# Performance work log

Hardware: AMD Instinct MI355X
Metric: run time of the kernel (lower is better)

The kernel has to match this reference:

```python
import jax, jax.numpy as jnp
import numpy as np

GRID = 18          # grid_dim
NTYPES = 6         # n_atom_types
SIGMA_P = 0.6      # sigma * bins_per_angstrom
B = 256            # number of environments (batch)
ATOMS_PER_ENV = 100
N = B * ATOMS_PER_ENV
EPS = 1e-5
SLOPE = 0.01       # LeakyReLU default negative slope


def _grid_points():
    # lin_spacing(): centers of 18 unit bins, -8.5 .. 8.5
    ls = np.linspace(-GRID / 2 + 0.5, GRID / 2 - 0.5, GRID)
    xx, yy, zz = np.meshgrid(ls, ls, ls, indexing='ij')
    return jnp.asarray(np.stack([xx, yy, zz], -1).reshape(-1, 3), jnp.float32)  # [G,3]


def _leaky(x):
    return jnp.where(x >= 0, x, SLOPE * x)


def _bn(x, g, b):
    # batch-norm with batch statistics (torch training-mode math), channel axis 1
    axes = tuple(i for i in range(x.ndim) if i != 1)
    m = x.mean(axes, keepdims=True)
    v = x.var(axes, keepdims=True)
    shp = [1] * x.ndim
    shp[1] = -1
    return (x - m) / jnp.sqrt(v + EPS) * g.reshape(shp) + b.reshape(shp)


def _conv3d(x, w, b, pad):
    y = jax.lax.conv_general_dilated(
        x, w, window_strides=(1, 1, 1), padding=[(pad, pad)] * 3,
        dimension_numbers=('NCDHW', 'OIDHW', 'NCDHW'))
    return y + b[None, :, None, None, None]


def _maxpool2(x):
    return jax.lax.reduce_window(x, -jnp.inf, jax.lax.max,
                                 (1, 1, 2, 2, 2), (1, 1, 2, 2, 2), 'VALID')


def _gaussian_blurring(pos, batch_ids, types):
    grid = _grid_points()                                  # [G,3], G=5832
    # squared distances via ||a-b||^2 = ||a||^2 + ||b||^2 - 2 a.b  -> avoids [G,N,3]
    d2 = (jnp.sum(grid * grid, -1)[:, None]
          + jnp.sum(pos * pos, -1)[None, :]
          - 2.0 * grid @ pos.T)                            # [G,N]
    dens = jnp.exp(-d2 / (2.0 * SIGMA_P ** 2))
    dens = dens / jnp.sum(dens, axis=0, keepdims=True)     # normalize per atom
    seg = batch_ids * NTYPES + types                       # [N]
    fields = jax.ops.segment_sum(dens.T, seg, num_segments=B * NTYPES)  # [B*6,G]
    return fields.reshape(B, NTYPES, GRID, GRID, GRID)


def setup_inputs() -> dict:
    key = jax.random.key(0)
    ks = jax.random.split(key, 16)
    pos = jax.random.uniform(ks[0], (N, 3), jnp.float32, -8.5, 8.5)
    batch_ids = jnp.repeat(jnp.arange(B, dtype=jnp.int32), ATOMS_PER_ENV)
    types = (jnp.arange(N, dtype=jnp.int32) % NTYPES)  # every env has every type
    s = 0.05
    return {
        'pos': pos,
        'c1w': jax.random.normal(ks[1], (16, 6, 3, 3, 3), jnp.float32) * s,
        'c1b': jax.random.normal(ks[2], (16,), jnp.float32) * s,
        'bn1g': jnp.ones((16,), jnp.float32), 'bn1b': jnp.zeros((16,), jnp.float32),
        'c2w': jax.random.normal(ks[3], (32, 16, 3, 3, 3), jnp.float32) * s,
        'c2b': jax.random.normal(ks[4], (32,), jnp.float32) * s,
        'bn2g': jnp.ones((32,), jnp.float32), 'bn2b': jnp.zeros((32,), jnp.float32),
        'c3w': jax.random.normal(ks[5], (64, 32, 3, 3, 3), jnp.float32) * s,
        'c3b': jax.random.normal(ks[6], (64,), jnp.float32) * s,
        'bn3g': jnp.ones((64,), jnp.float32), 'bn3b': jnp.zeros((64,), jnp.float32),
        'd1w': jax.random.normal(ks[7], (128, 64), jnp.float32) * s,
        'd1b': jax.random.normal(ks[8], (128,), jnp.float32) * s,
        'bn4g': jnp.ones((128,), jnp.float32), 'bn4b': jnp.zeros((128,), jnp.float32),
        'd2w': jax.random.normal(ks[9], (100, 128), jnp.float32) * s,
        'd2b': jax.random.normal(ks[10], (100,), jnp.float32) * s,
        'd3w': jax.random.normal(ks[11], (20, 100), jnp.float32) * s,
        'd3b': jax.random.normal(ks[12], (20,), jnp.float32) * s,
        'batch_ids': batch_ids,
        'types': types,
    }


def reference(pos, c1w, c1b, bn1g, bn1b, c2w, c2b, bn2g, bn2b, c3w, c3b, bn3g, bn3b,
              d1w, d1b, bn4g, bn4b, d2w, d2b, d3w, d3b, batch_ids, types):
    x = _gaussian_blurring(pos, batch_ids, types)            # [B,6,18,18,18]
    x = _leaky(_bn(_maxpool2(_conv3d(x, c1w, c1b, 1)), bn1g, bn1b))  # [B,16,9,9,9]
    x = _leaky(_bn(_maxpool2(_conv3d(x, c2w, c2b, 0)), bn2g, bn2b))  # [B,32,3,3,3]
    x = _leaky(_bn(_maxpool2(_conv3d(x, c3w, c3b, 1)), bn3g, bn3b))  # [B,64,1,1,1]
    x = x.reshape(x.shape[0], -1)                            # [B,64]
    x = _leaky(_bn(x @ d1w.T + d1b, bn4g, bn4b))             # [B,128]
    x = x @ d2w.T + d2b                                      # [B,100]
    x = _leaky(x)
    x = x @ d3w.T + d3b                                      # [B,20]
    return x
```

## Files before the change

kernel.cpp:

```cpp
#include <hip/hip_runtime.h>


#define G2 324
#define G3 5832
#define NT 6
#define BATCH 256
#define APE 100
#define EPS 1e-5f

typedef unsigned short u16;
typedef unsigned int u32;
typedef _Float16 h2 __attribute__((ext_vector_type(2)));

__device__ __forceinline__ float leaky(float x) { return x >= 0.0f ? x : 0.01f * x; }
__device__ __forceinline__ u32 pkh(float a, float b) {
    h2 v; v[0] = (_Float16)a; v[1] = (_Float16)b;
    return __builtin_bit_cast(u32, v);
}
__device__ __forceinline__ float fdot2u(u32 a, u32 b, float c) {
#if __has_builtin(__builtin_amdgcn_fdot2)
    return __builtin_amdgcn_fdot2(__builtin_bit_cast(h2, a),
                                  __builtin_bit_cast(h2, b), c, false);
#else
    h2 x = __builtin_bit_cast(h2, a), y = __builtin_bit_cast(h2, b);
    return c + (float)x[0] * (float)y[0] + (float)x[1] * (float)y[1];
#endif
}

__global__ __launch_bounds__(512) void k_splat(const float* __restrict__ pos,
        const int* __restrict__ types, u32* __restrict__ fields) {
    __shared__ float ew[APE * 54];
    __shared__ float ssum[APE * 3];
    __shared__ int list[APE];
    __shared__ int base[NT + 1];
    __shared__ int cnt[NT], cur[NT];
    const int b = blockIdx.x, tid = threadIdx.x;

    if (tid < NT) { cnt[tid] = 0; cur[tid] = 0; }
    __syncthreads();
    if (tid < APE) atomicAdd(&cnt[types[b * APE + tid]], 1);
    if (tid < 300) {
        const int la = tid / 3, ax = tid % 3;
        const float p = pos[(b * APE + la) * 3 + ax];
        float s = 0.0f;
        #pragma unroll
        for (int g = 0; g < 18; ++g) {
            const float d = (float)g - 8.5f - p;
            const float e = __expf(d * d * (-1.0f / 0.72f));
            ew[la * 54 + ax * 18 + g] = e;
            s += e;
        }
        ssum[tid] = s;
    }
    __syncthreads();
    if (tid == 0) {
        int s = 0;
        #pragma unroll
        for (int t = 0; t < NT; ++t) { base[t] = s; s += cnt[t]; }
        base[NT] = s;
    }
    if (tid < APE) {
        const float inv = 1.0f / (ssum[tid * 3] * ssum[tid * 3 + 1] * ssum[tid * 3 + 2]);
        #pragma unroll
        for (int g = 0; g < 18; ++g) ew[tid * 54 + g] *= inv;
    }
    __syncthreads();
    if (tid < APE) {
        const int t = types[b * APE + tid];
        const int j = atomicAdd(&cur[t], 1);
        list[base[t] + j] = tid;
    }
    __syncthreads();

    for (int it = tid; it < NT * 324; it += 512) {
        const int t = it / 324, r = it - t * 324;
        const int i = r / 18, j = r % 18;
        float acc[18];
        #pragma unroll
        for (int k = 0; k < 18; ++k) acc[k] = 0.0f;
        const int e1 = base[t + 1];
        for (int u = base[t]; u < e1; ++u) {
            const int a = list[u];
            const float exy = ew[a * 54 + i] * ew[a * 54 + 18 + j];
            const float* ez = &ew[a * 54 + 36];
            #pragma unroll
            for (int k = 0; k < 18; ++k) acc[k] += exy * ez[k];
        }
        u32* dst = &fields[((size_t)b * NT + t) * 2916 + (size_t)r * 9];
        #pragma unroll
        for (int q = 0; q < 9; ++q) dst[q] = pkh(acc[2 * q], acc[2 * q + 1]);
    }
}

template <int ZG>
__device__ __forceinline__ void conv1_pass(int c2, int Xl, int Yv, int b, int Xg,
        const u32* fldH, const u32* wpk, float* s_sum, float* s_ssq,
        const float* __restrict__ bias, float* __restrict__ a1) {
    float acc[2][2][2][6];
    #pragma unroll
    for (int c = 0; c < 2; ++c)
        #pragma unroll
        for (int o = 0; o < 2; ++o)
            #pragma unroll
            for (int p = 0; p < 2; ++p)
                #pragma unroll
                for (int z = 0; z < 6; ++z) acc[c][o][p][z] = 0.0f;

    for (int ic = 0; ic < 6; ++ic) {
        u32 A0[9], A1[9], Be0[9], Be1[9];
        #pragma unroll
        for (int d2 = 0; d2 < 9; ++d2) {
            const int wb = ((ic * 9 + d2) * 8 + c2) * 3;
            A0[d2] = wpk[wb]; A1[d2] = wpk[wb + 1];
            const u32 w2 = wpk[wb + 2];
            Be0[d2] = w2 & 0xFFFFu; Be1[d2] = w2 >> 16;
        }
        #pragma unroll
        for (int lj = 0; lj < 4; ++lj) {
            const int iy = 2 * Yv + lj - 1;
            const bool yok = (iy >= 0 && iy < 18);
            #pragma unroll
            for (int li = 0; li < 4; ++li) {
                const int ixl = 2 * Xl + li;
                u32 V[5], Sh[4];
                if (yok) {
                    const u32* rp = &fldH[((ic * 8 + ixl) * 18 + iy) * 10];
                    if (ZG == 0) {
                        V[0] = 0u;
                        #pragma unroll
                        for (int q = 0; q < 4; ++q) V[q + 1] = rp[q];
                    } else {
                        #pragma unroll
                        for (int q = 0; q < 5; ++q) V[q] = rp[3 * ZG - 1 + q];
                    }
                } else {
                    #pragma unroll
                    for (int q = 0; q < 5; ++q) V[q] = 0u;
                }
                #pragma unroll
                for (int q = 0; q < 4; ++q)
                    Sh[q] = __builtin_amdgcn_alignbit(V[q + 1], V[q], 16);
                #pragma unroll
                for (int o = 0; o < 2; ++o) {
                    const int dx = li - o;
                    if (dx < 0 || dx > 2) continue;
                    #pragma unroll
                    for (int p = 0; p < 2; ++p) {
                        const int dy = lj - p;
                        if (dy < 0 || dy > 2) continue;
                        const int d2 = dx * 3 + dy;
                        #pragma unroll
                        for (int ozl = 0; ozl < 6; ++ozl) {
                            if (ozl & 1) {
                                const int vi = (ozl - 1) / 2 + 1;
                                acc[0][o][p][ozl] = fdot2u(A0[d2], V[vi],
                                    fdot2u(Be0[d2], V[vi + 1], acc[0][o][p][ozl]));
                                acc[1][o][p][ozl] = fdot2u(A1[d2], V[vi],
                                    fdot2u(Be1[d2], V[vi + 1], acc[1][o][p][ozl]));
                            } else {
                                const int si = ozl / 2;
                                acc[0][o][p][ozl] = fdot2u(A0[d2], Sh[si],
                                    fdot2u(Be0[d2], Sh[si + 1], acc[0][o][p][ozl]));
                                acc[1][o][p][ozl] = fdot2u(A1[d2], Sh[si],
                                    fdot2u(Be1[d2], Sh[si + 1], acc[1][o][p][ozl]));
                            }
                        }
                    }
                }
            }
        }
    }
    const float bb0 = bias[2 * c2], bb1 = bias[2 * c2 + 1];
    float s0 = 0.0f, q0 = 0.0f, s1 = 0.0f, q1 = 0.0f;
    #pragma unroll
    for (int Zp = 0; Zp < 3; ++Zp) {
        float m0 = acc[0][0][0][2 * Zp], m1 = acc[1][0][0][2 * Zp];
        #pragma unroll
        for (int o = 0; o < 2; ++o)
            #pragma unroll
            for (int p = 0; p < 2; ++p) {
                m0 = fmaxf(m0, fmaxf(acc[0][o][p][2 * Zp], acc[0][o][p][2 * Zp + 1]));
                m1 = fmaxf(m1, fmaxf(acc[1][o][p][2 * Zp], acc[1][o][p][2 * Zp + 1]));
            }
        float2 vv; vv.x = m0 + bb0; vv.y = m1 + bb1;
        s0 += vv.x; q0 += vv.x * vv.x; s1 += vv.y; q1 += vv.y * vv.y;
        const int spg = (3 * Xg + Xl) * 81 + Yv * 9 + 3 * ZG + Zp;
        *(float2*)&a1[((size_t)b * 729 + spg) * 16 + 2 * c2] = vv;
    }
    atomicAdd(&s_sum[2 * c2], s0);     atomicAdd(&s_ssq[2 * c2], q0);
    atomicAdd(&s_sum[2 * c2 + 1], s1); atomicAdd(&s_ssq[2 * c2 + 1], q1);
}

__global__ __launch_bounds__(256, 3) void k_conv1(const u32* __restrict__ fields,
        const float* __restrict__ w, const float* __restrict__ bias,
        float* __restrict__ a1, float* __restrict__ stO) {
    __shared__ u32 fldH[48 * 18 * 10];
    __shared__ u32 wpk[432 * 3];
    __shared__ float s_sum[16], s_ssq[16];
    const int bx = blockIdx.x, b = bx / 3, Xg = bx % 3, tid = threadIdx.x;

    for (int i = tid; i < 432; i += 256) {
        const int c2 = i & 7, t = i >> 3, d2 = t % 9, ic = t / 9;
        const int w0 = (2 * c2) * 162 + ic * 27 + d2 * 3;
        const int w1 = w0 + 162;
        wpk[i * 3]     = pkh(w[w0], w[w0 + 1]);
        wpk[i * 3 + 1] = pkh(w[w1], w[w1 + 1]);
        wpk[i * 3 + 2] = pkh(w[w0 + 2], w[w1 + 2]);
    }
    if (tid < 16) { s_sum[tid] = 0.0f; s_ssq[tid] = 0.0f; }
    for (int i = tid; i < 8640; i += 256) {
        const int p = i % 10, t = i / 10;
        const int iy = t % 18, a = t / 18;
        const int ix = 6 * Xg - 1 + (a & 7);
        u32 v = 0;
        if (p < 9 && ix >= 0 && ix < 18)
            v = fields[((size_t)(b * 6 + (a >> 3)) * 324 + ix * 18 + iy) * 9 + p];
        fldH[t * 10 + p] = v;
    }
    __syncthreads();

    const int c2 = tid & 7, sp = tid >> 3;
    if (tid < 216) {
        const int Xl = sp / 9, Yv = sp % 9;
        conv1_pass<0>(c2, Xl, Yv, b, Xg, fldH, wpk, s_sum, s_ssq, bias, a1);
        conv1_pass<1>(c2, Xl, Yv, b, Xg, fldH, wpk, s_sum, s_ssq, bias, a1);
        conv1_pass<2>(c2, Xl, Yv, b, Xg, fldH, wpk, s_sum, s_ssq, bias, a1);
    }
    __syncthreads();
    if (tid < 16) { atomicAdd(&stO[tid], s_sum[tid]); atomicAdd(&stO[16 + tid], s_ssq[tid]); }
}

__global__ __launch_bounds__(576) void k_conv2(const float* __restrict__ a1,
        const float* __restrict__ w, const float* __restrict__ bias,
        const float* __restrict__ bng, const float* __restrict__ bnb,
        const float* __restrict__ stI, float* __restrict__ a2,
        float* __restrict__ stO) {
    __shared__ float xin[16 * 729];
    __shared__ float ws2[13824];
    __shared__ float sc[16], sh[16];
    __shared__ float s_sum[32], s_ssq[32];
    const int b = blockIdx.x, tid = threadIdx.x;
    if (tid < 16) {
        const float cnt = 256.0f * 729.0f;
        float m = stI[tid] / cnt;
        float v = stI[16 + tid] / cnt - m * m;
        float s = bng[tid] * rsqrtf(fmaxf(v, 0.0f) + EPS);
        sc[tid] = s; sh[tid] = bnb[tid] - m * s;
    }
    if (tid < 32) { s_sum[tid] = 0.0f; s_ssq[tid] = 0.0f; }
    __syncthreads();
    const float* src = a1 + (size_t)b * 729 * 16;
    for (int i = tid; i < 16 * 729; i += 576) {
        const int spb = i >> 4, c = i & 15;
        xin[c * 729 + spb] = leaky(src[i] * sc[c] + sh[c]);
    }
    for (int i = tid; i < 13824; i += 576) ws2[i] = w[i];
    __syncthreads();
    {
        const int oyi = tid & 1, oxi = (tid >> 1) & 1, rest = tid >> 2;
        const int Y = rest % 3, X = (rest / 3) % 3, c2 = rest / 9;
        const int ox = 2 * X + oxi, oy = 2 * Y + oyi;
        const int c0 = 2 * c2, c1 = c0 + 1;
        float acc0[6], acc1[6];
        #pragma unroll
        for (int z = 0; z < 6; ++z) { acc0[z] = 0.0f; acc1[z] = 0.0f; }
        for (int ic = 0; ic < 16; ++ic) {
            #pragma unroll
            for (int dx = 0; dx < 3; ++dx) {
                const int ix = ox + dx;
                #pragma unroll
                for (int dy = 0; dy < 3; ++dy) {
                    const int iy = oy + dy;
                    const float* rp = &xin[ic * 729 + ix * 81 + iy * 9];
                    float row[9];
                    #pragma unroll
                    for (int z = 0; z < 9; ++z) row[z] = rp[z];
                    const int wb0 = (c0 * 16 + ic) * 27 + dx * 9 + dy * 3;
                    const int wb1 = (c1 * 16 + ic) * 27 + dx * 9 + dy * 3;
                    #pragma unroll
                    for (int dz = 0; dz < 3; ++dz) {
                        const float w0 = ws2[wb0 + dz];
                        const float w1v = ws2[wb1 + dz];
                        #pragma unroll
                        for (int z = 0; z < 6; ++z) {
                            acc0[z] += w0 * row[z + dz];
                            acc1[z] += w1v * row[z + dz];
                        }
                    }
                }
            }
        }
        float pl[2][3];
        #pragma unroll
        for (int Z = 0; Z < 3; ++Z) {
            float v0 = fmaxf(acc0[2 * Z], acc0[2 * Z + 1]);
            float v1 = fmaxf(acc1[2 * Z], acc1[2 * Z + 1]);
            v0 = fmaxf(v0, __shfl_xor(v0, 1)); v0 = fmaxf(v0, __shfl_xor(v0, 2));
            v1 = fmaxf(v1, __shfl_xor(v1, 1)); v1 = fmaxf(v1, __shfl_xor(v1, 2));
            pl[0][Z] = v0; pl[1][Z] = v1;
        }
        if ((tid & 3) == 0) {
            #pragma unroll
            for (int hh = 0; hh < 2; ++hh) {
                const int c = c0 + hh;
                const float bb = bias[c];
                float s0 = 0.0f, q0 = 0.0f;
                #pragma unroll
                for (int Z = 0; Z < 3; ++Z) {
                    const float v = pl[hh][Z] + bb;
                    a2[((size_t)b * 32 + c) * 27 + X * 9 + Y * 3 + Z] = v;
                    s0 += v; q0 += v * v;
                }
                atomicAdd(&s_sum[c], s0); atomicAdd(&s_ssq[c], q0);
            }
        }
    }
    __syncthreads();
    if (tid < 32) { atomicAdd(&stO[tid], s_sum[tid]); atomicAdd(&stO[32 + tid], s_ssq[tid]); }
}

__global__ __launch_bounds__(256) void k_conv3(const float* __restrict__ a2,
        const float* __restrict__ w, const float* __restrict__ bias,
        const float* __restrict__ bng, const float* __restrict__ bnb,
        const float* __restrict__ stI, float* __restrict__ a3,
        float* __restrict__ stO) {
    __shared__ float x[864];
    __shared__ float pacc[256 * 8];
    __shared__ float sc[32], sh[32];
    const int b = blockIdx.x, tid = threadIdx.x;
    if (tid < 32) {
        const float cnt = 256.0f * 27.0f;
        float m = stI[tid] / cnt;
        float v = stI[32 + tid] / cnt - m * m;
        float s = bng[tid] * rsqrtf(fmaxf(v, 0.0f) + EPS);
        sc[tid] = s; sh[tid] = bnb[tid] - m * s;
    }
    __syncthreads();
    for (int i = tid; i < 864; i += 256) {
        int c = i / 27;
        x[i] = leaky(a2[(size_t)b * 864 + i] * sc[c] + sh[c]);
    }
    __syncthreads();
    const int c = tid & 63, q = tid >> 6;
    float acc[8];
    #pragma unroll
    for (int p = 0; p < 8; ++p) acc[p] = 0.0f;
    for (int ic = q * 8; ic < q * 8 + 8; ++ic) {
        const float* wr = w + ((size_t)c * 32 + ic) * 27;
        #pragma unroll
        for (int d = 0; d < 27; ++d) {
            const int dx = d / 9, dy = (d / 3) % 3, dz = d % 3;
            const float wv = wr[d];
            #pragma unroll
            for (int p = 0; p < 8; ++p) {
                const int px = p >> 2, py = (p >> 1) & 1, pz = p & 1;
                const int ix = px + dx - 1, iy = py + dy - 1, iz = pz + dz - 1;
                if (ix >= 0 && iy >= 0 && iz >= 0)
                    acc[p] += wv * x[ic * 27 + ix * 9 + iy * 3 + iz];
            }
        }
    }
    #pragma unroll
    for (int p = 0; p < 8; ++p) pacc[tid * 8 + p] = acc[p];
    __syncthreads();
    if (q == 0) {
        float m = -1e30f;
        #pragma unroll
        for (int p = 0; p < 8; ++p) {
            float v = pacc[c * 8 + p] + pacc[(64 + c) * 8 + p]
                    + pacc[(128 + c) * 8 + p] + pacc[(192 + c) * 8 + p];
            m = fmaxf(m, v);
        }
        float v = m + bias[c];
        a3[(size_t)b * 64 + c] = v;
        atomicAdd(&stO[c], v); atomicAdd(&stO[64 + c], v * v);
    }
}

__global__ __launch_bounds__(128) void k_dense1(const float* __restrict__ a3,
        const float* __restrict__ bng, const float* __restrict__ bnb,
        const float* __restrict__ stI,
        const float* __restrict__ w1, const float* __restrict__ b1,
        float* __restrict__ h1, float* __restrict__ stO) {
    __shared__ float x[64];
    const int b = blockIdx.x, tid = threadIdx.x;
    if (tid < 64) {
        float m = stI[tid] / 256.0f;
        float v = stI[64 + tid] / 256.0f - m * m;
        float s = bng[tid] * rsqrtf(fmaxf(v, 0.0f) + EPS);
        x[tid] = leaky(a3[(size_t)b * 64 + tid] * s + (bnb[tid] - m * s));
    }
    __syncthreads();
    const float* wr = w1 + tid * 64;
    float acc = b1[tid];
    #pragma unroll
    for (int i = 0; i < 64; ++i) acc += x[i] * wr[i];
    h1[(size_t)b * 128 + tid] = acc;
    atomicAdd(&stO[tid], acc); atomicAdd(&stO[128 + tid], acc * acc);
}

__global__ __launch_bounds__(128) void k_dense2(const float* __restrict__ h1,
        const float* __restrict__ bng, const float* __restrict__ bnb,
        const float* __restrict__ stI,
        const float* __restrict__ w2, const float* __restrict__ bias2,
        const float* __restrict__ w3, const float* __restrict__ bias3,
        float* __restrict__ out) {
    __shared__ float x[128];
    __shared__ float y[100];
    const int b = blockIdx.x, tid = threadIdx.x;
    {
        float m = stI[tid] / 256.0f;
        float v = stI[128 + tid] / 256.0f - m * m;
        float s = bng[tid] * rsqrtf(fmaxf(v, 0.0f) + EPS);
        x[tid] = leaky(h1[(size_t)b * 128 + tid] * s + (bnb[tid] - m * s));
    }
    __syncthreads();
    if (tid < 100) {
        const float* wr = w2 + tid * 128;
        float acc = bias2[tid];
        #pragma unroll
        for (int i = 0; i < 128; ++i) acc += x[i] * wr[i];
        y[tid] = leaky(acc);
    }
    __syncthreads();
    if (tid < 20) {
        const float* wr = w3 + tid * 100;
        float acc = bias3[tid];
        #pragma unroll
        for (int i = 0; i < 100; ++i) acc += y[i] * wr[i];
        out[(size_t)b * 20 + tid] = acc;
    }
}

extern "C" void kernel_launch(void* const* d_in, const int* in_sizes, int n_in,
                              void* d_out, int out_size, void* d_ws, size_t ws_size,
                              hipStream_t stream) {
    (void)in_sizes; (void)n_in; (void)out_size; (void)ws_size;
    const float* pos  = (const float*)d_in[0];
    const float* c1w  = (const float*)d_in[1];
    const float* c1b  = (const float*)d_in[2];
    const float* bn1g = (const float*)d_in[3];
    const float* bn1b = (const float*)d_in[4];
    const float* c2w  = (const float*)d_in[5];
    const float* c2b  = (const float*)d_in[6];
    const float* bn2g = (const float*)d_in[7];
    const float* bn2b = (const float*)d_in[8];
    const float* c3w  = (const float*)d_in[9];
    const float* c3b  = (const float*)d_in[10];
    const float* bn3g = (const float*)d_in[11];
    const float* bn3b = (const float*)d_in[12];
    const float* d1w  = (const float*)d_in[13];
    const float* d1b  = (const float*)d_in[14];
    const float* bn4g = (const float*)d_in[15];
    const float* bn4b = (const float*)d_in[16];
    const float* d2w  = (const float*)d_in[17];
    const float* d2b  = (const float*)d_in[18];
    const float* d3w  = (const float*)d_in[19];
    const float* d3b  = (const float*)d_in[20];
    const int* types  = (const int*)d_in[22];

    float* ws = (float*)d_ws;
    float* st = ws;
    float* a3 = ws + 512;
    float* h1 = a3 + 16384;
    float* a2 = h1 + 32768;
    float* a1 = a2 + 221184;
    u32* fields = (u32*)(a1 + 2985984);

    hipMemsetAsync(st, 0, 480 * sizeof(float), stream);
    k_splat <<<BATCH, 512, 0, stream>>>(pos, types, fields);
    k_conv1 <<<3 * BATCH, 256, 0, stream>>>(fields, c1w, c1b, a1, st);
    k_conv2 <<<BATCH, 576, 0, stream>>>(a1, c2w, c2b, bn1g, bn1b, st, a2, st + 32);
    k_conv3 <<<BATCH, 256, 0, stream>>>(a2, c3w, c3b, bn2g, bn2b, st + 32, a3, st + 96);
    k_dense1<<<BATCH, 128, 0, stream>>>(a3, bn3g, bn3b, st + 96, d1w, d1b, h1, st + 224);
    k_dense2<<<BATCH, 128, 0, stream>>>(h1, bn4g, bn4b, st + 224, d2w, d2b, d3w, d3b,
                                        (float*)d_out);
}
```

Measured before the change: 236.8 us.

## Replace conv1 fdot2 inner loop with scalar fp16 FMAs and split conv2 by channel half

Conv1 stops using packed fdot2 with alignbit-shifted operands. It now unpacks fp16 values and does scalar float FMAs per tap, with a simpler weight layout (one packed pair per tap and channel pair) and a field row stride padded to 12. Out-of-range y rows are skipped with a branch instead of zero-filled. Conv2 is split into two blocks per batch element, each handling 16 output channels with half the weight staging, which doubles the grid and cuts shared memory per block. Conv1 roughly doubles its arithmetic instruction count by dropping dot2, in exchange for simpler register use.

```diff
diff --git a/kernel.cpp b/kernel.cpp
--- a/kernel.cpp
+++ b/kernel.cpp
@@ -16,15 +16,6 @@
 __device__ __forceinline__ u32 pkh(float a, float b) {
     h2 v; v[0] = (_Float16)a; v[1] = (_Float16)b;
     return __builtin_bit_cast(u32, v);
-}
-__device__ __forceinline__ float fdot2u(u32 a, u32 b, float c) {
-#if __has_builtin(__builtin_amdgcn_fdot2)
-    return __builtin_amdgcn_fdot2(__builtin_bit_cast(h2, a),
-                                  __builtin_bit_cast(h2, b), c, false);
-#else
-    h2 x = __builtin_bit_cast(h2, a), y = __builtin_bit_cast(h2, b);
-    return c + (float)x[0] * (float)y[0] + (float)x[1] * (float)y[1];
-#endif
 }
 
 __global__ __launch_bounds__(512) void k_splat(const float* __restrict__ pos,
@@ -107,24 +98,18 @@
                 for (int z = 0; z < 6; ++z) acc[c][o][p][z] = 0.0f;
 
     for (int ic = 0; ic < 6; ++ic) {
-        u32 A0[9], A1[9], Be0[9], Be1[9];
-        #pragma unroll
-        for (int d2 = 0; d2 < 9; ++d2) {
-            const int wb = ((ic * 9 + d2) * 8 + c2) * 3;
-            A0[d2] = wpk[wb]; A1[d2] = wpk[wb + 1];
-            const u32 w2 = wpk[wb + 2];
-            Be0[d2] = w2 & 0xFFFFu; Be1[d2] = w2 >> 16;
-        }
+        u32 wq[27];
+        #pragma unroll
+        for (int d = 0; d < 27; ++d) wq[d] = wpk[(ic * 27 + d) * 8 + c2];
         #pragma unroll
         for (int lj = 0; lj < 4; ++lj) {
             const int iy = 2 * Yv + lj - 1;
-            const bool yok = (iy >= 0 && iy < 18);
-            #pragma unroll
-            for (int li = 0; li < 4; ++li) {
-                const int ixl = 2 * Xl + li;
-                u32 V[5], Sh[4];
-                if (yok) {
-                    const u32* rp = &fldH[((ic * 8 + ixl) * 18 + iy) * 10];
+            if (iy >= 0 && iy < 18) {
+                #pragma unroll
+                for (int li = 0; li < 4; ++li) {
+                    const int ixl = 2 * Xl + li;
+                    const u32* rp = &fldH[((ic * 8 + ixl) * 18 + iy) * 12];
+                    u32 V[5];
                     if (ZG == 0) {
                         V[0] = 0u;
                         #pragma unroll
@@ -133,36 +118,27 @@
                         #pragma unroll
                         for (int q = 0; q < 5; ++q) V[q] = rp[3 * ZG - 1 + q];
                     }
-                } else {
                     #pragma unroll
-                    for (int q = 0; q < 5; ++q) V[q] = 0u;
-                }
-                #pragma unroll
-                for (int q = 0; q < 4; ++q)
-                    Sh[q] = __builtin_amdgcn_alignbit(V[q + 1], V[q], 16);
-                #pragma unroll
-                for (int o = 0; o < 2; ++o) {
-                    const int dx = li - o;
-                    if (dx < 0 || dx > 2) continue;
-                    #pragma unroll
-                    for (int p = 0; p < 2; ++p) {
-                        const int dy = lj - p;
-                        if (dy < 0 || dy > 2) continue;
-                        const int d2 = dx * 3 + dy;
+                    for (int o = 0; o < 2; ++o) {
+                        const int dx = li - o;
+                        if (dx < 0 || dx > 2) continue;
                         #pragma unroll
-                        for (int ozl = 0; ozl < 6; ++ozl) {
-                            if (ozl & 1) {
-                                const int vi = (ozl - 1) / 2 + 1;
-                                acc[0][o][p][ozl] = fdot2u(A0[d2], V[vi],
-                                    fdot2u(Be0[d2], V[vi + 1], acc[0][o][p][ozl]));
-                                acc[1][o][p][ozl] = fdot2u(A1[d2], V[vi],
-                                    fdot2u(Be1[d2], V[vi + 1], acc[1][o][p][ozl]));
-                            } else {
-                                const int si = ozl / 2;
-                                acc[0][o][p][ozl] = fdot2u(A0[d2], Sh[si],
-                                    fdot2u(Be0[d2], Sh[si + 1], acc[0][o][p][ozl]));
-                                acc[1][o][p][ozl] = fdot2u(A1[d2], Sh[si],
-                                    fdot2u(Be1[d2], Sh[si + 1], acc[1][o][p][ozl]));
+                        for (int p = 0; p < 2; ++p) {
+                            const int dy = lj - p;
+                            if (dy < 0 || dy > 2) continue;
+                            const int db = dx * 9 + dy * 3;
+                            #pragma unroll
+                            for (int dz = 0; dz < 3; ++dz) {
+                                const h2 wp = __builtin_bit_cast(h2, wq[db + dz]);
+                                #pragma unroll
+                                for (int oz = 0; oz < 6; ++oz) {
+                                    const int zl = oz + dz - 1;
+                                    const h2 rv = __builtin_bit_cast(h2,
+                                        V[(zl + 2) >> 1]);
+                                    const _Float16 r = rv[(zl + 2) & 1];
+                                    acc[0][o][p][oz] += (float)wp[0] * (float)r;
+                                    acc[1][o][p][oz] += (float)wp[1] * (float)r;
+                                }
                             }
                         }
                     }
@@ -194,28 +170,25 @@
 __global__ __launch_bounds__(256, 3) void k_conv1(const u32* __restrict__ fields,
         const float* __restrict__ w, const float* __restrict__ bias,
         float* __restrict__ a1, float* __restrict__ stO) {
-    __shared__ u32 fldH[48 * 18 * 10];
-    __shared__ u32 wpk[432 * 3];
+    __shared__ u32 fldH[48 * 18 * 12];
+    __shared__ u32 wpk[6 * 27 * 8];
     __shared__ float s_sum[16], s_ssq[16];
     const int bx = blockIdx.x, b = bx / 3, Xg = bx % 3, tid = threadIdx.x;
 
-    for (int i = tid; i < 432; i += 256) {
-        const int c2 = i & 7, t = i >> 3, d2 = t % 9, ic = t / 9;
-        const int w0 = (2 * c2) * 162 + ic * 27 + d2 * 3;
-        const int w1 = w0 + 162;
-        wpk[i * 3]     = pkh(w[w0], w[w0 + 1]);
-        wpk[i * 3 + 1] = pkh(w[w1], w[w1 + 1]);
-        wpk[i * 3 + 2] = pkh(w[w0 + 2], w[w1 + 2]);
+    for (int i = tid; i < 1296; i += 256) {
+        const int c2 = i & 7, t = i >> 3, d = t % 27, ic = t / 27;
+        const int w0 = (2 * c2) * 162 + ic * 27 + d;
+        wpk[(ic * 27 + d) * 8 + c2] = pkh(w[w0], w[w0 + 162]);
     }
     if (tid < 16) { s_sum[tid] = 0.0f; s_ssq[tid] = 0.0f; }
-    for (int i = tid; i < 8640; i += 256) {
-        const int p = i % 10, t = i / 10;
+    for (int i = tid; i < 48 * 18 * 12; i += 256) {
+        const int p = i % 12, t = i / 12;
         const int iy = t % 18, a = t / 18;
         const int ix = 6 * Xg - 1 + (a & 7);
         u32 v = 0;
         if (p < 9 && ix >= 0 && ix < 18)
             v = fields[((size_t)(b * 6 + (a >> 3)) * 324 + ix * 18 + iy) * 9 + p];
-        fldH[t * 10 + p] = v;
+        fldH[i] = v;
     }
     __syncthreads();
 
@@ -230,37 +203,37 @@
     if (tid < 16) { atomicAdd(&stO[tid], s_sum[tid]); atomicAdd(&stO[16 + tid], s_ssq[tid]); }
 }
 
-__global__ __launch_bounds__(576) void k_conv2(const float* __restrict__ a1,
+__global__ __launch_bounds__(320) void k_conv2(const float* __restrict__ a1,
         const float* __restrict__ w, const float* __restrict__ bias,
         const float* __restrict__ bng, const float* __restrict__ bnb,
         const float* __restrict__ stI, float* __restrict__ a2,
         float* __restrict__ stO) {
     __shared__ float xin[16 * 729];
-    __shared__ float ws2[13824];
+    __shared__ float ws2[6912];
     __shared__ float sc[16], sh[16];
-    __shared__ float s_sum[32], s_ssq[32];
-    const int b = blockIdx.x, tid = threadIdx.x;
+    __shared__ float s_sum[16], s_ssq[16];
+    const int bx = blockIdx.x, b = bx >> 1, half = bx & 1, tid = threadIdx.x;
     if (tid < 16) {
         const float cnt = 256.0f * 729.0f;
         float m = stI[tid] / cnt;
         float v = stI[16 + tid] / cnt - m * m;
         float s = bng[tid] * rsqrtf(fmaxf(v, 0.0f) + EPS);
         sc[tid] = s; sh[tid] = bnb[tid] - m * s;
-    }
-    if (tid < 32) { s_sum[tid] = 0.0f; s_ssq[tid] = 0.0f; }
+        s_sum[tid] = 0.0f; s_ssq[tid] = 0.0f;
+    }
     __syncthreads();
     const float* src = a1 + (size_t)b * 729 * 16;
-    for (int i = tid; i < 16 * 729; i += 576) {
+    for (int i = tid; i < 16 * 729; i += 320) {
         const int spb = i >> 4, c = i & 15;
         xin[c * 729 + spb] = leaky(src[i] * sc[c] + sh[c]);
     }
-    for (int i = tid; i < 13824; i += 576) ws2[i] = w[i];
-    __syncthreads();
-    {
+    for (int i = tid; i < 6912; i += 320) ws2[i] = w[half * 6912 + i];
+    __syncthreads();
+    if (tid < 288) {
         const int oyi = tid & 1, oxi = (tid >> 1) & 1, rest = tid >> 2;
         const int Y = rest % 3, X = (rest / 3) % 3, c2 = rest / 9;
         const int ox = 2 * X + oxi, oy = 2 * Y + oyi;
-        const int c0 = 2 * c2, c1 = c0 + 1;
+        const int cl0 = 2 * c2, cl1 = cl0 + 1;
         float acc0[6], acc1[6];
         #pragma unroll
         for (int z = 0; z < 6; ++z) { acc0[z] = 0.0f; acc1[z] = 0.0f; }
@@ -275,8 +248,8 @@
                     float row[9];
                     #pragma unroll
                     for (int z = 0; z < 9; ++z) row[z] = rp[z];
-                    const int wb0 = (c0 * 16 + ic) * 27 + dx * 9 + dy * 3;
-                    const int wb1 = (c1 * 16 + ic) * 27 + dx * 9 + dy * 3;
+                    const int wb0 = (cl0 * 16 + ic) * 27 + dx * 9 + dy * 3;
+                    const int wb1 = (cl1 * 16 + ic) * 27 + dx * 9 + dy * 3;
                     #pragma unroll
                     for (int dz = 0; dz < 3; ++dz) {
                         const float w0 = ws2[wb0 + dz];
@@ -302,7 +275,7 @@
         if ((tid & 3) == 0) {
             #pragma unroll
             for (int hh = 0; hh < 2; ++hh) {
-                const int c = c0 + hh;
+                const int cl = cl0 + hh, c = half * 16 + cl;
                 const float bb = bias[c];
                 float s0 = 0.0f, q0 = 0.0f;
                 #pragma unroll
@@ -311,12 +284,15 @@
                     a2[((size_t)b * 32 + c) * 27 + X * 9 + Y * 3 + Z] = v;
                     s0 += v; q0 += v * v;
                 }
-                atomicAdd(&s_sum[c], s0); atomicAdd(&s_ssq[c], q0);
+                atomicAdd(&s_sum[cl], s0); atomicAdd(&s_ssq[cl], q0);
             }
         }
     }
     __syncthreads();
-    if (tid < 32) { atomicAdd(&stO[tid], s_sum[tid]); atomicAdd(&stO[32 + tid], s_ssq[tid]); }
+    if (tid < 16) {
+        const int c = half * 16 + tid;
+        atomicAdd(&stO[c], s_sum[tid]); atomicAdd(&stO[32 + c], s_ssq[tid]);
+    }
 }
 
 __global__ __launch_bounds__(256) void k_conv3(const float* __restrict__ a2,
@@ -470,7 +446,7 @@
     hipMemsetAsync(st, 0, 480 * sizeof(float), stream);
     k_splat <<<BATCH, 512, 0, stream>>>(pos, types, fields);
     k_conv1 <<<3 * BATCH, 256, 0, stream>>>(fields, c1w, c1b, a1, st);
-    k_conv2 <<<BATCH, 576, 0, stream>>>(a1, c2w, c2b, bn1g, bn1b, st, a2, st + 32);
+    k_conv2 <<<2 * BATCH, 320, 0, stream>>>(a1, c2w, c2b, bn1g, bn1b, st, a2, st + 32);
     k_conv3 <<<BATCH, 256, 0, stream>>>(a2, c3w, c3b, bn2g, bn2b, st + 32, a3, st + 96);
     k_dense1<<<BATCH, 128, 0, stream>>>(a3, bn3g, bn3b, st + 96, d1w, d1b, h1, st + 224);
     k_dense2<<<BATCH, 128, 0, stream>>>(h1, bn4g, bn4b, st + 224, d2w, d2b, d3w, d3b,
```

Result: slower. 695.7 us (+193.8%).
